# Optimization experiments

Hardware: AMD Instinct MI355X
Metric: run time of the kernel (lower is better)

The kernel has to match this reference:

```python
import jax, jax.numpy as jnp
import numpy as np

DIM = 1024

def setup_inputs() -> dict:
    key = jax.random.key(0)
    ks = jax.random.split(key, 7)
    s = 1.0 / np.sqrt(DIM)
    x = jax.random.normal(ks[0], (8, 2048, DIM), dtype=jnp.float32)
    Wq = jax.random.uniform(ks[1], (DIM, DIM), jnp.float32, -s, s)
    bq = jax.random.uniform(ks[2], (DIM,), jnp.float32, -s, s)
    Wk = jax.random.uniform(ks[3], (DIM, DIM), jnp.float32, -s, s)
    bk = jax.random.uniform(ks[4], (DIM,), jnp.float32, -s, s)
    Wv = jax.random.uniform(ks[5], (DIM, DIM), jnp.float32, -s, s)
    bv = jax.random.uniform(ks[6], (DIM,), jnp.float32, -s, s)
    return {"x": x, "Wq": Wq, "bq": bq, "Wk": Wk, "bk": bk, "Wv": Wv, "bv": bv}

def reference(x, Wq, bq, Wk, bk, Wv, bv):
    # nn.Linear: y = x @ W.T + b
    q = jnp.einsum('bsd,ed->bse', x, Wq) + bq  # [B,S,D]
    k = jnp.einsum('bsd,ed->bse', x, Wk) + bk
    v = jnp.einsum('bsd,ed->bse', x, Wv) + bv
    scores = jnp.einsum('bqd,bkd->bqk', q, k) / jnp.sqrt(jnp.float32(DIM))
    attn = jax.nn.softmax(scores, axis=-1)
    return jnp.einsum('bqk,bkd->bqd', attn, v)
```

## Files before the change

### kernel.cpp

```cpp
#include <hip/hip_runtime.h>

#define DIM 1024
#define SEQ 2048

typedef __attribute__((ext_vector_type(8))) short bf16x8;
typedef __attribute__((ext_vector_type(4))) float f32x4;
typedef __attribute__((ext_vector_type(4))) unsigned short us4;
typedef __attribute__((ext_vector_type(4))) _Float16 h4;

__device__ __forceinline__ unsigned short f2bf(float f) {
    union { float f; unsigned int u; } v; v.f = f;
    unsigned int r = (v.u + 0x7FFFu + ((v.u >> 16) & 1u)) >> 16;
    return (unsigned short)r;
}

#define GLOAD(gp, lp) __builtin_amdgcn_global_load_lds( \
    (const __attribute__((address_space(1))) unsigned int*)(gp), \
    (__attribute__((address_space(3))) unsigned int*)(lp), 16, 0, 0)

__global__ __launch_bounds__(256) void cast_f32_bf16(const float* __restrict__ src,
                                                     unsigned short* __restrict__ dst, int n) {
    int i = (blockIdx.x * 256 + threadIdx.x) * 8;
    if (i >= n) return;
    float4 a = *(const float4*)(src + i);
    float4 b = *(const float4*)(src + i + 4);
    us4 lo = { f2bf(a.x), f2bf(a.y), f2bf(a.z), f2bf(a.w) };
    us4 hi = { f2bf(b.x), f2bf(b.y), f2bf(b.z), f2bf(b.w) };
    *(us4*)(dst + i) = lo;
    *(us4*)(dst + i + 4) = hi;
}

#define STAGE(buf, op, q, G, ld, kt) \
    GLOAD((G) + (size_t)((q) * 128 + lr) * (ld) + (kt) + csrc, \
          smem + (buf) * 32768 + (op) * 16384 + (q) * 8192 + wid * 1024)

__device__ __forceinline__ void gemm256_core(
    const unsigned short* __restrict__ A, const unsigned short* __restrict__ B,
    int lda, int ldb, int K, char* smem, f32x4 acc[8][4])
{
    const int tid = threadIdx.x;
    const int lane = tid & 63;
    const int wid = tid >> 6;
    const int wm = wid >> 2;
    const int wn = wid & 3;
    const int lr = tid >> 2;
    const int csrc = ((tid & 3) ^ ((tid >> 3) & 3)) * 8;

    const int niter = K >> 7;

#pragma unroll
    for (int jb = 0; jb < 3; jb++) {
        STAGE(jb, 0, 0, A, lda, jb * 32); STAGE(jb, 0, 1, A, lda, jb * 32);
        STAGE(jb, 1, 0, B, ldb, jb * 32); STAGE(jb, 1, 1, B, ldb, jb * 32);
    }
    asm volatile("s_waitcnt vmcnt(8)" ::: "memory");
    __builtin_amdgcn_s_barrier();

    for (int it = 0; it < niter; ++it) {
        bf16x8 bfr[4];
#pragma unroll
        for (int p = 0; p < 8; ++p) {
            const int j = p >> 1;
            const int mh = p & 1;
            bf16x8 af[4];
#pragma unroll
            for (int mi = 0; mi < 4; mi++) {
                int row = wm * 128 + mh * 64 + mi * 16 + (lane & 15);
                int cr = (lane >> 4) ^ ((row >> 1) & 3);
                af[mi] = *(const bf16x8*)(smem + j * 32768 + row * 64 + cr * 16);
            }
            if (mh == 0) {
#pragma unroll
                for (int nj = 0; nj < 4; nj++) {
                    int row = wn * 64 + nj * 16 + (lane & 15);
                    int cr = (lane >> 4) ^ ((row >> 1) & 3);
                    bfr[nj] = *(const bf16x8*)(smem + j * 32768 + 16384 + row * 64 + cr * 16);
                }
            }
            {
                int skt = it * 128 + (j + 3) * 32;
                if (skt < K) {
                    int sb = (j + 3) & 3;
                    if (mh == 0) { STAGE(sb, 0, 0, A, lda, skt); STAGE(sb, 0, 1, A, lda, skt); }
                    else         { STAGE(sb, 1, 0, B, ldb, skt); STAGE(sb, 1, 1, B, ldb, skt); }
                }
            }
            __builtin_amdgcn_s_barrier();
            __builtin_amdgcn_s_setprio(1);
#pragma unroll
            for (int mi = 0; mi < 4; mi++)
#pragma unroll
                for (int nj = 0; nj < 4; nj++)
                    acc[mh * 4 + mi][nj] =
                        __builtin_amdgcn_mfma_f32_16x16x32_bf16(af[mi], bfr[nj], acc[mh * 4 + mi][nj], 0, 0, 0);
            __builtin_amdgcn_s_setprio(0);
            if (mh == 1) asm volatile("s_waitcnt vmcnt(8)" ::: "memory");
            __builtin_amdgcn_s_barrier();
        }
    }
}

#define ACC_INIT() \
    f32x4 acc[8][4]; \
    _Pragma("unroll") for (int i = 0; i < 8; i++) \
    _Pragma("unroll") for (int jj = 0; jj < 4; jj++) acc[i][jj] = (f32x4){0.f, 0.f, 0.f, 0.f};

__global__ __launch_bounds__(512, 2) void gemm_qkv(
    const unsigned short* __restrict__ xb, const unsigned short* __restrict__ wb,
    const float* __restrict__ bq, const float* __restrict__ bk, const float* __restrict__ bv,
    unsigned short* __restrict__ qb, unsigned short* __restrict__ kb, unsigned short* __restrict__ vt)
{
    extern __shared__ char smem[];
    const int bz = blockIdx.z;
    const int m0 = blockIdx.y * 256, n0 = blockIdx.x * 256;
    const float* bias = (bz == 0) ? bq : ((bz == 1) ? bk : bv);
    ACC_INIT();
    gemm256_core(xb + (size_t)m0 * DIM, wb + (size_t)bz * DIM * DIM + (size_t)n0 * DIM,
                 DIM, DIM, DIM, smem, acc);
    const int lane = threadIdx.x & 63, wid = threadIdx.x >> 6;
    const int wm = wid >> 2, wn = wid & 3;
    const float scale = (bz == 0) ? 0.03125f : 1.0f;
    unsigned short* C = (bz == 0) ? qb : kb;
#pragma unroll
    for (int mig = 0; mig < 8; mig++)
#pragma unroll
        for (int nj = 0; nj < 4; nj++) {
            int col = n0 + wn * 64 + nj * 16 + (lane & 15);
            float bcol = bias[col];
#pragma unroll
            for (int r = 0; r < 4; r++) {
                int row = m0 + wm * 128 + mig * 16 + (lane >> 4) * 4 + r;
                float v = (acc[mig][nj][r] + bcol) * scale;
                if (bz < 2) {
                    C[(size_t)row * DIM + col] = f2bf(v);
                } else {
                    int b = row >> 11, s = row & 2047;
                    vt[((size_t)b << 21) + ((size_t)col << 11) + s] = f2bf(v);
                }
            }
        }
}

__global__ __launch_bounds__(512, 2) void gemm_qk(
    const unsigned short* __restrict__ qb, const unsigned short* __restrict__ kb,
    unsigned short* __restrict__ sb)
{
    extern __shared__ char smem[];
    const int b = blockIdx.z;
    const int m0 = blockIdx.y * 256, n0 = blockIdx.x * 256;
    ACC_INIT();
    gemm256_core(qb + ((size_t)b * SEQ + m0) * DIM, kb + ((size_t)b * SEQ + n0) * DIM,
                 DIM, DIM, DIM, smem, acc);
    const int lane = threadIdx.x & 63, wid = threadIdx.x >> 6;
    const int wm = wid >> 2, wn = wid & 3;
    _Float16* sh = (_Float16*)sb + (size_t)b * SEQ * SEQ;
#pragma unroll
    for (int mig = 0; mig < 8; mig++)
#pragma unroll
        for (int nj = 0; nj < 4; nj++) {
            int col = n0 + wn * 64 + nj * 16 + (lane & 15);
#pragma unroll
            for (int r = 0; r < 4; r++) {
                int row = m0 + wm * 128 + mig * 16 + (lane >> 4) * 4 + r;
                sh[(size_t)row * SEQ + col] = (_Float16)acc[mig][nj][r];
            }
        }
}

__global__ __launch_bounds__(256) void softmax_p(unsigned short* __restrict__ sb)
{
    const int lane = threadIdx.x & 63, wid = threadIdx.x >> 6;
    const size_t row = (size_t)blockIdx.x * 4 + wid;
    unsigned short* rp = sb + row * SEQ;
    float v[32];
#pragma unroll
    for (int j = 0; j < 8; j++) {
        h4 h = *(const h4*)(rp + (j * 64 + lane) * 4);
#pragma unroll
        for (int e = 0; e < 4; e++) v[j * 4 + e] = (float)h[e];
    }
    float m = -1e30f;
#pragma unroll
    for (int i = 0; i < 32; i++) m = fmaxf(m, v[i]);
#pragma unroll
    for (int msk = 1; msk <= 32; msk <<= 1) m = fmaxf(m, __shfl_xor(m, msk, 64));
    float s = 0.f;
#pragma unroll
    for (int i = 0; i < 32; i++) { v[i] = __expf(v[i] - m); s += v[i]; }
#pragma unroll
    for (int msk = 1; msk <= 32; msk <<= 1) s += __shfl_xor(s, msk, 64);
    float inv = 1.0f / s;
#pragma unroll
    for (int j = 0; j < 8; j++) {
        us4 pu = { f2bf(v[j * 4] * inv), f2bf(v[j * 4 + 1] * inv),
                   f2bf(v[j * 4 + 2] * inv), f2bf(v[j * 4 + 3] * inv) };
        *(us4*)(rp + (j * 64 + lane) * 4) = pu;
    }
}

__global__ __launch_bounds__(512, 2) void gemm_pv(
    const unsigned short* __restrict__ pb, const unsigned short* __restrict__ vt,
    float* __restrict__ out)
{
    extern __shared__ char smem[];
    const int b = blockIdx.z;
    const int m0 = blockIdx.y * 256, n0 = blockIdx.x * 256;
    ACC_INIT();
    gemm256_core(pb + ((size_t)b * SEQ + m0) * SEQ, vt + ((size_t)b * DIM + n0) * SEQ,
                 SEQ, SEQ, SEQ, smem, acc);
    const int lane = threadIdx.x & 63, wid = threadIdx.x >> 6;
    const int wm = wid >> 2, wn = wid & 3;
    float* O = out + (size_t)b * SEQ * DIM;
#pragma unroll
    for (int mig = 0; mig < 8; mig++)
#pragma unroll
        for (int nj = 0; nj < 4; nj++) {
            int col = n0 + wn * 64 + nj * 16 + (lane & 15);
#pragma unroll
            for (int r = 0; r < 4; r++) {
                int row = m0 + wm * 128 + mig * 16 + (lane >> 4) * 4 + r;
                O[(size_t)row * DIM + col] = acc[mig][nj][r];
            }
        }
}

extern "C" void kernel_launch(void* const* d_in, const int* in_sizes, int n_in,
                              void* d_out, int out_size, void* d_ws, size_t ws_size,
                              hipStream_t stream) {
    const float* x  = (const float*)d_in[0];
    const float* Wq = (const float*)d_in[1];
    const float* bq = (const float*)d_in[2];
    const float* Wk = (const float*)d_in[3];
    const float* bk = (const float*)d_in[4];
    const float* Wv = (const float*)d_in[5];
    const float* bv = (const float*)d_in[6];
    float* out = (float*)d_out;
    char* ws = (char*)d_ws;

    unsigned short* xb = (unsigned short*)(ws);
    unsigned short* wb = (unsigned short*)(ws + 33554432);
    unsigned short* qb = (unsigned short*)(ws + 39845888);
    unsigned short* kb = (unsigned short*)(ws + 73400320);
    unsigned short* vt = (unsigned short*)(ws + 106954752);
    unsigned short* sb = (unsigned short*)(ws + 140509184);

    cast_f32_bf16<<<dim3(8192), 256, 0, stream>>>(x, xb, 16777216);
    cast_f32_bf16<<<dim3(512), 256, 0, stream>>>(Wq, wb, 1048576);
    cast_f32_bf16<<<dim3(512), 256, 0, stream>>>(Wk, wb + 1048576, 1048576);
    cast_f32_bf16<<<dim3(512), 256, 0, stream>>>(Wv, wb + 2097152, 1048576);

    hipFuncSetAttribute((const void*)gemm_qkv, hipFuncAttributeMaxDynamicSharedMemorySize, 131072);
    hipFuncSetAttribute((const void*)gemm_qk,  hipFuncAttributeMaxDynamicSharedMemorySize, 131072);
    hipFuncSetAttribute((const void*)gemm_pv,  hipFuncAttributeMaxDynamicSharedMemorySize, 131072);

    gemm_qkv<<<dim3(4, 64, 3), 512, 131072, stream>>>(xb, wb, bq, bk, bv, qb, kb, vt);
    gemm_qk<<<dim3(8, 8, 8), 512, 131072, stream>>>(qb, kb, sb);
    softmax_p<<<dim3(4096), 256, 0, stream>>>(sb);
    gemm_pv<<<dim3(4, 8, 8), 512, 131072, stream>>>(sb, vt, out);
}
```

Baseline: 331.3 us.

## Restructure GEMM main loop to one barrier per K-step and remap blocks XCD-aware

Rewrites the GEMM core loop to process one 32-wide K phase per iteration. Each phase does a single waitcnt and barrier, loads all A/B fragments up front using precomputed LDS offsets, issues the next stage's four global-to-LDS loads, then runs 32 MFMAs. This replaces the previous two-barrier half-phase scheme. It also flattens the grids of all three GEMM kernels and remaps block ids so consecutive logical tiles land on the same XCD (bid&7 stride), aiming for better L2 reuse. The changes raise register pressure from holding 8 A fragments and alter the overlap between loads and compute.

```diff
diff --git a/kernel.cpp b/kernel.cpp
--- a/kernel.cpp
+++ b/kernel.cpp
@@ -30,9 +30,12 @@
     *(us4*)(dst + i + 4) = hi;
 }
 
-#define STAGE(buf, op, q, G, ld, kt) \
-    GLOAD((G) + (size_t)((q) * 128 + lr) * (ld) + (kt) + csrc, \
-          smem + (buf) * 32768 + (op) * 16384 + (q) * 8192 + wid * 1024)
+#define STAGE4(sb, kt) do { \
+    GLOAD(A + (size_t)(lr) * lda + (kt) + csrc,       smem + (sb) * 32768 + wid * 1024); \
+    GLOAD(A + (size_t)(128 + lr) * lda + (kt) + csrc, smem + (sb) * 32768 + 8192 + wid * 1024); \
+    GLOAD(B + (size_t)(lr) * ldb + (kt) + csrc,       smem + (sb) * 32768 + 16384 + wid * 1024); \
+    GLOAD(B + (size_t)(128 + lr) * ldb + (kt) + csrc, smem + (sb) * 32768 + 24576 + wid * 1024); \
+} while (0)
 
 __device__ __forceinline__ void gemm256_core(
     const unsigned short* __restrict__ A, const unsigned short* __restrict__ B,
@@ -46,57 +49,45 @@
     const int lr = tid >> 2;
     const int csrc = ((tid & 3) ^ ((tid >> 3) & 3)) * 8;
 
-    const int niter = K >> 7;
-
-#pragma unroll
-    for (int jb = 0; jb < 3; jb++) {
-        STAGE(jb, 0, 0, A, lda, jb * 32); STAGE(jb, 0, 1, A, lda, jb * 32);
-        STAGE(jb, 1, 0, B, ldb, jb * 32); STAGE(jb, 1, 1, B, ldb, jb * 32);
-    }
-    asm volatile("s_waitcnt vmcnt(8)" ::: "memory");
-    __builtin_amdgcn_s_barrier();
-
-    for (int it = 0; it < niter; ++it) {
-        bf16x8 bfr[4];
-#pragma unroll
-        for (int p = 0; p < 8; ++p) {
-            const int j = p >> 1;
-            const int mh = p & 1;
-            bf16x8 af[4];
-#pragma unroll
-            for (int mi = 0; mi < 4; mi++) {
-                int row = wm * 128 + mh * 64 + mi * 16 + (lane & 15);
-                int cr = (lane >> 4) ^ ((row >> 1) & 3);
-                af[mi] = *(const bf16x8*)(smem + j * 32768 + row * 64 + cr * 16);
-            }
-            if (mh == 0) {
-#pragma unroll
-                for (int nj = 0; nj < 4; nj++) {
-                    int row = wn * 64 + nj * 16 + (lane & 15);
-                    int cr = (lane >> 4) ^ ((row >> 1) & 3);
-                    bfr[nj] = *(const bf16x8*)(smem + j * 32768 + 16384 + row * 64 + cr * 16);
-                }
-            }
-            {
-                int skt = it * 128 + (j + 3) * 32;
-                if (skt < K) {
-                    int sb = (j + 3) & 3;
-                    if (mh == 0) { STAGE(sb, 0, 0, A, lda, skt); STAGE(sb, 0, 1, A, lda, skt); }
-                    else         { STAGE(sb, 1, 0, B, ldb, skt); STAGE(sb, 1, 1, B, ldb, skt); }
-                }
-            }
-            __builtin_amdgcn_s_barrier();
-            __builtin_amdgcn_s_setprio(1);
-#pragma unroll
-            for (int mi = 0; mi < 4; mi++)
-#pragma unroll
-                for (int nj = 0; nj < 4; nj++)
-                    acc[mh * 4 + mi][nj] =
-                        __builtin_amdgcn_mfma_f32_16x16x32_bf16(af[mi], bfr[nj], acc[mh * 4 + mi][nj], 0, 0, 0);
-            __builtin_amdgcn_s_setprio(0);
-            if (mh == 1) asm volatile("s_waitcnt vmcnt(8)" ::: "memory");
-            __builtin_amdgcn_s_barrier();
-        }
+    int aoff[8], boff[4];
+    {
+        int arow = wm * 128 + (lane & 15);
+        int cr = (lane >> 4) ^ ((arow >> 1) & 3);
+#pragma unroll
+        for (int mi = 0; mi < 8; mi++) aoff[mi] = (arow + mi * 16) * 64 + cr * 16;
+        int brow = wn * 64 + (lane & 15);
+        int crb = (lane >> 4) ^ ((brow >> 1) & 3);
+#pragma unroll
+        for (int nj = 0; nj < 4; nj++) boff[nj] = 16384 + (brow + nj * 16) * 64 + crb * 16;
+    }
+
+    const int nph = K >> 5;
+
+#pragma unroll
+    for (int jb = 0; jb < 3; jb++) STAGE4(jb, jb * 32);
+
+    for (int j = 0; j < nph; ++j) {
+        if (j + 2 < nph)      asm volatile("s_waitcnt vmcnt(8)" ::: "memory");
+        else if (j + 1 < nph) asm volatile("s_waitcnt vmcnt(4)" ::: "memory");
+        else                  asm volatile("s_waitcnt vmcnt(0)" ::: "memory");
+        __builtin_amdgcn_s_barrier();
+
+        const char* bufb = smem + (j & 3) * 32768;
+        bf16x8 af[8], bfr[4];
+#pragma unroll
+        for (int mi = 0; mi < 8; mi++) af[mi] = *(const bf16x8*)(bufb + aoff[mi]);
+#pragma unroll
+        for (int nj = 0; nj < 4; nj++) bfr[nj] = *(const bf16x8*)(bufb + boff[nj]);
+
+        if (j + 3 < nph) STAGE4((j + 3) & 3, (j + 3) * 32);
+
+        __builtin_amdgcn_s_setprio(1);
+#pragma unroll
+        for (int mi = 0; mi < 8; mi++)
+#pragma unroll
+            for (int nj = 0; nj < 4; nj++)
+                acc[mi][nj] = __builtin_amdgcn_mfma_f32_16x16x32_bf16(af[mi], bfr[nj], acc[mi][nj], 0, 0, 0);
+        __builtin_amdgcn_s_setprio(0);
     }
 }
 
@@ -111,8 +102,11 @@
     unsigned short* __restrict__ qb, unsigned short* __restrict__ kb, unsigned short* __restrict__ vt)
 {
     extern __shared__ char smem[];
-    const int bz = blockIdx.z;
-    const int m0 = blockIdx.y * 256, n0 = blockIdx.x * 256;
+    const int bid = blockIdx.x;
+    const int lb = (bid & 7) * 96 + (bid >> 3);
+    const int bz = lb >> 8;
+    const int r = lb & 255;
+    const int m0 = (r >> 2) * 256, n0 = (r & 3) * 256;
     const float* bias = (bz == 0) ? bq : ((bz == 1) ? bk : bv);
     ACC_INIT();
     gemm256_core(xb + (size_t)m0 * DIM, wb + (size_t)bz * DIM * DIM + (size_t)n0 * DIM,
@@ -128,9 +122,9 @@
             int col = n0 + wn * 64 + nj * 16 + (lane & 15);
             float bcol = bias[col];
 #pragma unroll
-            for (int r = 0; r < 4; r++) {
-                int row = m0 + wm * 128 + mig * 16 + (lane >> 4) * 4 + r;
-                float v = (acc[mig][nj][r] + bcol) * scale;
+            for (int rr = 0; rr < 4; rr++) {
+                int row = m0 + wm * 128 + mig * 16 + (lane >> 4) * 4 + rr;
+                float v = (acc[mig][nj][rr] + bcol) * scale;
                 if (bz < 2) {
                     C[(size_t)row * DIM + col] = f2bf(v);
                 } else {
@@ -146,8 +140,11 @@
     unsigned short* __restrict__ sb)
 {
     extern __shared__ char smem[];
-    const int b = blockIdx.z;
-    const int m0 = blockIdx.y * 256, n0 = blockIdx.x * 256;
+    const int bid = blockIdx.x;
+    const int lb = (bid & 7) * 64 + (bid >> 3);
+    const int b = lb >> 6;
+    const int r = lb & 63;
+    const int m0 = (r >> 3) * 256, n0 = (r & 7) * 256;
     ACC_INIT();
     gemm256_core(qb + ((size_t)b * SEQ + m0) * DIM, kb + ((size_t)b * SEQ + n0) * DIM,
                  DIM, DIM, DIM, smem, acc);
@@ -160,9 +157,9 @@
         for (int nj = 0; nj < 4; nj++) {
             int col = n0 + wn * 64 + nj * 16 + (lane & 15);
 #pragma unroll
-            for (int r = 0; r < 4; r++) {
-                int row = m0 + wm * 128 + mig * 16 + (lane >> 4) * 4 + r;
-                sh[(size_t)row * SEQ + col] = (_Float16)acc[mig][nj][r];
+            for (int rr = 0; rr < 4; rr++) {
+                int row = m0 + wm * 128 + mig * 16 + (lane >> 4) * 4 + rr;
+                sh[(size_t)row * SEQ + col] = (_Float16)acc[mig][nj][rr];
             }
         }
 }
@@ -203,8 +200,11 @@
     float* __restrict__ out)
 {
     extern __shared__ char smem[];
-    const int b = blockIdx.z;
-    const int m0 = blockIdx.y * 256, n0 = blockIdx.x * 256;
+    const int bid = blockIdx.x;
+    const int lb = (bid & 7) * 32 + (bid >> 3);
+    const int b = lb >> 5;
+    const int r = lb & 31;
+    const int m0 = (r >> 2) * 256, n0 = (r & 3) * 256;
     ACC_INIT();
     gemm256_core(pb + ((size_t)b * SEQ + m0) * SEQ, vt + ((size_t)b * DIM + n0) * SEQ,
                  SEQ, SEQ, SEQ, smem, acc);
@@ -217,9 +217,9 @@
         for (int nj = 0; nj < 4; nj++) {
             int col = n0 + wn * 64 + nj * 16 + (lane & 15);
 #pragma unroll
-            for (int r = 0; r < 4; r++) {
-                int row = m0 + wm * 128 + mig * 16 + (lane >> 4) * 4 + r;
-                O[(size_t)row * DIM + col] = acc[mig][nj][r];
+            for (int rr = 0; rr < 4; rr++) {
+                int row = m0 + wm * 128 + mig * 16 + (lane >> 4) * 4 + rr;
+                O[(size_t)row * DIM + col] = acc[mig][nj][rr];
             }
         }
 }
@@ -253,8 +253,8 @@
     hipFuncSetAttribute((const void*)gemm_qk,  hipFuncAttributeMaxDynamicSharedMemorySize, 131072);
     hipFuncSetAttribute((const void*)gemm_pv,  hipFuncAttributeMaxDynamicSharedMemorySize, 131072);
 
-    gemm_qkv<<<dim3(4, 64, 3), 512, 131072, stream>>>(xb, wb, bq, bk, bv, qb, kb, vt);
-    gemm_qk<<<dim3(8, 8, 8), 512, 131072, stream>>>(qb, kb, sb);
+    gemm_qkv<<<dim3(768), 512, 131072, stream>>>(xb, wb, bq, bk, bv, qb, kb, vt);
+    gemm_qk<<<dim3(512), 512, 131072, stream>>>(qb, kb, sb);
     softmax_p<<<dim3(4096), 256, 0, stream>>>(sb);
-    gemm_pv<<<dim3(4, 8, 8), 512, 131072, stream>>>(sb, vt, out);
-}
+    gemm_pv<<<dim3(256), 512, 131072, stream>>>(sb, vt, out);
+}
```

After: 350.6 us. 1.06x slower.
